# Performance work log

Measured on AMD Instinct MI355X. Metric: run time of the kernel, lower is better.

Reference implementation:

```python
import jax, jax.numpy as jnp
import numpy as np

B, D, H, DH, DFF = 2, 1024, 16, 64, 4096
NB, NR, S = 24, 8, 512
SCALE_DEPTH = 1.4
FSQ_DIM, FSQ_LEVELS = 32, 8
EPS = 1e-5


def rmsnorm(x, w):
    var = jnp.mean(x * x, axis=-1, keepdims=True)
    return x * jax.lax.rsqrt(var + EPS) * w


def rope_cos_sin(position):
    # position: [B] int -> cos/sin [B, DH/2]
    inv = 1.0 / (10000.0 ** (jnp.arange(0, DH, 2, dtype=jnp.float32) / DH))
    ang = position.astype(jnp.float32)[:, None] * inv[None, :]
    return jnp.cos(ang), jnp.sin(ang)


def apply_rope(x, cos, sin):
    # x: [B, H, 1, DH]
    x1, x2 = jnp.split(x, 2, axis=-1)
    c = cos[:, None, None, :]
    s = sin[:, None, None, :]
    return jnp.concatenate([x1 * c - x2 * s, x1 * s + x2 * c], axis=-1)


def run_lm(hidden, cache_k, cache_v, params, cos, sin, n_layers):
    # hidden [B,1,D]; cache_k/v [L,B,H,S,DH]; params: stacked per-layer weights.
    scale = SCALE_DEPTH / np.sqrt(n_layers)  # MuP residual scale
    inv_sqrt_dh = 1.0 / np.sqrt(DH)

    def body(h, xs):
        ln1, wq, wk, wv, wo, ln2, wg, wu, wd, ck, cv = xs
        res = h
        hn = rmsnorm(h, ln1)
        q = (hn @ wq).reshape(B, 1, H, DH).transpose(0, 2, 1, 3)
        k = (hn @ wk).reshape(B, 1, H, DH).transpose(0, 2, 1, 3)
        v = (hn @ wv).reshape(B, 1, H, DH).transpose(0, 2, 1, 3)
        q = apply_rope(q, cos, sin)
        k = apply_rope(k, cos, sin)
        nk = jnp.concatenate([ck, k], axis=2)  # [B,H,S+1,DH]
        nv = jnp.concatenate([cv, v], axis=2)
        att = jnp.einsum('bhqd,bhkd->bhqk', q, nk) * inv_sqrt_dh
        p = jax.nn.softmax(att, axis=-1)
        o = jnp.einsum('bhqk,bhkd->bhqd', p, nv).transpose(0, 2, 1, 3).reshape(B, 1, D) @ wo
        h = res + o * scale
        res = h
        hn = rmsnorm(h, ln2)
        mlp = (jax.nn.silu(hn @ wg) * (hn @ wu)) @ wd
        h = res + mlp * scale
        return h, (nk, nv)

    ln1, wq, wk, wv, wo, ln2, wg, wu, wd = params
    hidden, (nk, nv) = jax.lax.scan(
        body, hidden, (ln1, wq, wk, wv, wo, ln2, wg, wu, wd, cache_k, cache_v))
    return hidden, nk, nv


def fsq(x, w_in, w_out):
    # finite scalar quantization with straight-through rounding
    z = jnp.tanh(x @ w_in)
    half = (FSQ_LEVELS - 1) / 2.0
    zq = jnp.round(z * half) / half
    zq = z + jax.lax.stop_gradient(zq - z)
    return zq @ w_out


def _forward(position, embed, base_k, base_v, res_k, res_v,
             base_ln1, base_ln2, base_wq, base_wk, base_wv, base_wo,
             base_wg, base_wu, base_wd, base_norm,
             res_ln1, res_ln2, res_wq, res_wk, res_wv, res_wo,
             res_wg, res_wu, res_wd, res_norm,
             fsq_in, fsq_out, stop_proj_w, stop_proj_b, stop_head_w, stop_head_b):
    cos, sin = rope_cos_sin(position)
    hidden, bnk, bnv = run_lm(
        embed, base_k, base_v,
        (base_ln1, base_wq, base_wk, base_wv, base_wo, base_ln2, base_wg, base_wu, base_wd),
        cos, sin, NB)
    lm_hidden = rmsnorm(hidden, base_norm)
    lm_fsq = fsq(lm_hidden, fsq_in, fsq_out)
    stop_logit = jax.nn.silu(lm_hidden @ stop_proj_w + stop_proj_b) @ stop_head_w + stop_head_b
    res_in = lm_fsq + embed
    rh, rnk, rnv = run_lm(
        res_in, res_k, res_v,
        (res_ln1, res_wq, res_wk, res_wv, res_wo, res_ln2, res_wg, res_wu, res_wd),
        cos, sin, NR)
    rh = rmsnorm(rh, res_norm)
    return (lm_fsq, rh, stop_logit, bnk, bnv, rnk, rnv)


def setup_inputs() -> dict:
    key = jax.random.key(0)
    ks = iter(jax.random.split(key, 40))

    def p(shape, scale=0.02):
        return jax.random.normal(next(ks), shape, dtype=jnp.float32) * scale

    return {
        'embed': jax.random.normal(next(ks), (B, 1, D), jnp.float32),
        'position': jax.random.randint(next(ks), (B,), 0, S),
        'base_k': jax.random.normal(next(ks), (NB, B, H, S, DH), jnp.float32),
        'base_v': jax.random.normal(next(ks), (NB, B, H, S, DH), jnp.float32),
        'res_k': jax.random.normal(next(ks), (NR, B, H, S, DH), jnp.float32),
        'res_v': jax.random.normal(next(ks), (NR, B, H, S, DH), jnp.float32),
        'base_ln1': jnp.ones((NB, D), jnp.float32),
        'base_ln2': jnp.ones((NB, D), jnp.float32),
        'base_wq': p((NB, D, D)), 'base_wk': p((NB, D, D)),
        'base_wv': p((NB, D, D)), 'base_wo': p((NB, D, D)),
        'base_wg': p((NB, D, DFF)), 'base_wu': p((NB, D, DFF)), 'base_wd': p((NB, DFF, D)),
        'base_norm': jnp.ones((D,), jnp.float32),
        'res_ln1': jnp.ones((NR, D), jnp.float32),
        'res_ln2': jnp.ones((NR, D), jnp.float32),
        'res_wq': p((NR, D, D)), 'res_wk': p((NR, D, D)),
        'res_wv': p((NR, D, D)), 'res_wo': p((NR, D, D)),
        'res_wg': p((NR, D, DFF)), 'res_wu': p((NR, D, DFF)), 'res_wd': p((NR, DFF, D)),
        'res_norm': jnp.ones((D,), jnp.float32),
        'fsq_in': p((D, FSQ_DIM)), 'fsq_out': p((FSQ_DIM, D)),
        'stop_proj_w': p((D, D)), 'stop_proj_b': jnp.zeros((D,), jnp.float32),
        'stop_head_w': p((D, 1)), 'stop_head_b': jnp.zeros((1,), jnp.float32),
    }


def reference(embed, position, base_k, base_v, res_k, res_v,
              base_ln1, base_ln2, base_wq, base_wk, base_wv, base_wo,
              base_wg, base_wu, base_wd, base_norm,
              res_ln1, res_ln2, res_wq, res_wk, res_wv, res_wo,
              res_wg, res_wu, res_wd, res_norm,
              fsq_in, fsq_out, stop_proj_w, stop_proj_b, stop_head_w, stop_head_b):
    return _forward(position, embed, base_k, base_v, res_k, res_v,
                    base_ln1, base_ln2, base_wq, base_wk, base_wv, base_wo,
                    base_wg, base_wu, base_wd, base_norm,
                    res_ln1, res_ln2, res_wq, res_wk, res_wv, res_wo,
                    res_wg, res_wu, res_wd, res_norm,
                    fsq_in, fsq_out, stop_proj_w, stop_proj_b, stop_head_w, stop_head_b)
```

## Files before the change

kernel.cpp:

```cpp
#include <hip/hip_runtime.h>
#include <cmath>

#define D 1024
#define DFF 4096
#define NHEADS 16
#define DH 64
#define S_CACHE 512
#define SP1 513
#define NB_L 24
#define NR_L 8
#define NCH 17

#define WS_H      0
#define WS_H2     2048
#define WS_QKV    4096
#define WS_ATTN   102400
#define WS_OPROJ  139392
#define WS_GU     155776
#define WS_DOWN   286848
#define WS_SPROJ  303232

__device__ __forceinline__ float silu(float x) { return x / (1.f + expf(-x)); }

__device__ __forceinline__ void prologue_norm(
    const float* __restrict__ hbase,
    const float* __restrict__ part, int nks, float scale,
    const float* __restrict__ lnw,
    float (*hn)[D], float* __restrict__ hout)
{
  __shared__ float redw[4];
  const int t = threadIdx.x;
  const int b = t >> 7;
  const int i0 = (t & 127) * 8;
  const float4* hb4 = (const float4*)(hbase + b * D + i0);
  const float4 h0 = hb4[0], h1 = hb4[1];
  float acc[8] = {h0.x, h0.y, h0.z, h0.w, h1.x, h1.y, h1.z, h1.w};
  if (part != nullptr) {
    float s[8] = {0,0,0,0,0,0,0,0};
    for (int ks = 0; ks < nks; ++ks) {
      const float4* p4 = (const float4*)(part + (size_t)(ks * 2 + b) * D + i0);
      const float4 a = p4[0], c = p4[1];
      s[0]+=a.x; s[1]+=a.y; s[2]+=a.z; s[3]+=a.w;
      s[4]+=c.x; s[5]+=c.y; s[6]+=c.z; s[7]+=c.w;
    }
#pragma unroll
    for (int u = 0; u < 8; ++u) acc[u] += scale * s[u];
  }
  float ssq = 0.f;
#pragma unroll
  for (int u = 0; u < 8; ++u) ssq += acc[u] * acc[u];
#pragma unroll
  for (int off = 32; off; off >>= 1) ssq += __shfl_xor(ssq, off);
  if ((t & 63) == 0) redw[t >> 6] = ssq;
  __syncthreads();
  const float r = rsqrtf((redw[b * 2] + redw[b * 2 + 1]) * (1.f / D) + 1e-5f);
#pragma unroll
  for (int u = 0; u < 8; ++u) hn[b][i0 + u] = acc[u] * r * lnw[i0 + u];
  if (hout != nullptr && blockIdx.x == 0 && blockIdx.y == 0) {
    float4* o4 = (float4*)(hout + b * D + i0);
    o4[0] = make_float4(acc[0], acc[1], acc[2], acc[3]);
    o4[1] = make_float4(acc[4], acc[5], acc[6], acc[7]);
  }
  __syncthreads();
}

__global__ __launch_bounds__(256) void k_qkv(
    const float* __restrict__ hbase, const float* __restrict__ down_part,
    float* __restrict__ hout, const float* __restrict__ ln1,
    const float* __restrict__ wq, const float* __restrict__ wk,
    const float* __restrict__ wv,
    float* __restrict__ qkv_part, float scale, int has_prev)
{
  __shared__ float hn[2][D];
  __shared__ float redg[16][2][64];
  const int t = threadIdx.x;
  const int ks = blockIdx.x;
  const int cg = blockIdx.y;
  const int mat = cg >> 4;
  const int jbase = (cg & 15) * 64;
  const float* W = (mat == 0) ? wq : (mat == 1) ? wk : wv;
  const int jo4 = (t & 15) * 4;
  const int kp = t >> 4;
  const int ib = ks * 64 + kp * 4;
  float4 wbuf[4];
#pragma unroll
  for (int r = 0; r < 4; ++r)
    wbuf[r] = *(const float4*)(W + (size_t)(ib + r) * D + jbase + jo4);
  prologue_norm(hbase, has_prev ? down_part : nullptr, 8, scale, ln1, hn, hout);
  float a00=0,a01=0,a02=0,a03=0, a10=0,a11=0,a12=0,a13=0;
#pragma unroll
  for (int r = 0; r < 4; ++r) {
    const float x0 = hn[0][ib + r], x1 = hn[1][ib + r];
    a00 += wbuf[r].x*x0; a01 += wbuf[r].y*x0; a02 += wbuf[r].z*x0; a03 += wbuf[r].w*x0;
    a10 += wbuf[r].x*x1; a11 += wbuf[r].y*x1; a12 += wbuf[r].z*x1; a13 += wbuf[r].w*x1;
  }
  redg[kp][0][jo4+0]=a00; redg[kp][0][jo4+1]=a01; redg[kp][0][jo4+2]=a02; redg[kp][0][jo4+3]=a03;
  redg[kp][1][jo4+0]=a10; redg[kp][1][jo4+1]=a11; redg[kp][1][jo4+2]=a12; redg[kp][1][jo4+3]=a13;
  __syncthreads();
  if (t < 128) {
    const int b = t >> 6, jo = t & 63;
    float s = 0.f;
#pragma unroll
    for (int k2 = 0; k2 < 16; ++k2) s += redg[k2][b][jo];
    qkv_part[(size_t)((ks * 3 + mat) * 2 + b) * D + jbase + jo] = s;
  }
}

__global__ __launch_bounds__(256) void k_attn(
    const float* __restrict__ qkv_part, const int* __restrict__ position,
    const float* __restrict__ k_in, const float* __restrict__ v_in,
    float* __restrict__ k_out, float* __restrict__ v_out,
    float* __restrict__ attn_part)
{
  const int t = threadIdx.x;
  const int chunk = blockIdx.x;
  const int bh = blockIdx.y;
  const int b = bh >> 4, h = bh & 15;
  __shared__ float q[64];
  __shared__ float sc[32];
  __shared__ float red8[8][32];
  __shared__ float pvred[16][64];
  __shared__ float mlsh[2];
  __shared__ float kn[64], vn[64];
  const size_t row_in  = (size_t)bh * S_CACHE;
  const size_t row_out = (size_t)bh * SP1;
  const int pbase = (bh * NCH + chunk) * 68;

  if (chunk < 16) {
    const float4* ksrc = (const float4*)(k_in + (row_in + chunk * 32) * 64);
    float4*       kdst = (float4*)(k_out + (row_out + chunk * 32) * 64);
    const float4* vsrc = (const float4*)(v_in + (row_in + chunk * 32) * 64);
    float4*       vdst = (float4*)(v_out + (row_out + chunk * 32) * 64);
    const float4 kc0 = ksrc[t], kc1 = ksrc[t + 256];
    const float4 vc0 = vsrc[t], vc1 = vsrc[t + 256];
    kdst[t] = kc0; kdst[t + 256] = kc1;
    vdst[t] = vc0; vdst[t + 256] = vc1;
    if (t < 64) {
      float s = 0.f;
#pragma unroll
      for (int ks = 0; ks < 16; ++ks)
        s += qkv_part[(size_t)(ks * 6 + b) * D + h * 64 + t];
      q[t] = s;
    }
    __syncthreads();
    if (t < 32) {
      const float pos = (float)position[b];
      const float inv = expf(-(float)t * 0.28782313662425575f);
      const float ang = pos * inv;
      const float c = cosf(ang), sn = sinf(ang);
      const float x1 = q[t], x2 = q[t + 32];
      q[t]      = (x1 * c - x2 * sn) * 0.125f;
      q[t + 32] = (x1 * sn + x2 * c) * 0.125f;
    }
    __syncthreads();
    {
      const int key = t & 31, kp = t >> 5;
      const float* krow = k_in + (row_in + chunk * 32 + key) * 64 + kp * 8;
      const float4 k0 = *(const float4*)krow;
      const float4 k1 = *(const float4*)(krow + 4);
      const int d = kp * 8;
      float dp = k0.x*q[d] + k0.y*q[d+1] + k0.z*q[d+2] + k0.w*q[d+3]
               + k1.x*q[d+4] + k1.y*q[d+5] + k1.z*q[d+6] + k1.w*q[d+7];
      red8[kp][key] = dp;
    }
    __syncthreads();
    if (t < 32) {
      float score = 0.f;
#pragma unroll
      for (int k2 = 0; k2 < 8; ++k2) score += red8[k2][t];
      float m = score;
#pragma unroll
      for (int off = 16; off; off >>= 1) m = fmaxf(m, __shfl_xor(m, off));
      const float p = expf(score - m);
      float l = p;
#pragma unroll
      for (int off = 16; off; off >>= 1) l += __shfl_xor(l, off);
      sc[t] = p;
      if (t == 0) { mlsh[0] = m; mlsh[1] = l; }
    }
    __syncthreads();
    {
      const int d4 = (t & 15) * 4, sp = t >> 4;
      float ax = 0.f, ay = 0.f, az = 0.f, aw = 0.f;
#pragma unroll
      for (int r = 0; r < 2; ++r) {
        const int sl = sp * 2 + r;
        const float4 vv = *(const float4*)(v_in + (row_in + chunk * 32 + sl) * 64 + d4);
        const float p2 = sc[sl];
        ax += vv.x * p2; ay += vv.y * p2; az += vv.z * p2; aw += vv.w * p2;
      }
      pvred[sp][d4+0]=ax; pvred[sp][d4+1]=ay; pvred[sp][d4+2]=az; pvred[sp][d4+3]=aw;
    }
    __syncthreads();
    if (t < 64) {
      float a = 0.f;
#pragma unroll
      for (int s2 = 0; s2 < 16; ++s2) a += pvred[s2][t];
      attn_part[pbase + 2 + t] = a;
      if (t == 0) { attn_part[pbase + 0] = mlsh[0]; attn_part[pbase + 1] = mlsh[1]; }
    }
  } else {
    if (t < 64) {
      float skv = 0.f, svv = 0.f;
#pragma unroll
      for (int ks = 0; ks < 16; ++ks) {
        skv += qkv_part[(size_t)(ks * 6 + 2 + b) * D + h * 64 + t];
        svv += qkv_part[(size_t)(ks * 6 + 4 + b) * D + h * 64 + t];
      }
      kn[t] = skv; vn[t] = svv;
    }
    if (t < 64) {
      float s = 0.f;
#pragma unroll
      for (int ks = 0; ks < 16; ++ks)
        s += qkv_part[(size_t)(ks * 6 + b) * D + h * 64 + t];
      q[t] = s;
    }
    __syncthreads();
    if (t < 32) {
      const float pos = (float)position[b];
      const float inv = expf(-(float)t * 0.28782313662425575f);
      const float ang = pos * inv;
      const float c = cosf(ang), sn = sinf(ang);
      float x1 = kn[t], x2 = kn[t + 32];
      kn[t]      = x1 * c - x2 * sn;
      kn[t + 32] = x1 * sn + x2 * c;
      x1 = q[t]; x2 = q[t + 32];
      q[t]      = (x1 * c - x2 * sn) * 0.125f;
      q[t + 32] = (x1 * sn + x2 * c) * 0.125f;
    }
    __syncthreads();
    if (t < 64) {
      k_out[(row_out + S_CACHE) * 64 + t] = kn[t];
      v_out[(row_out + S_CACHE) * 64 + t] = vn[t];
      float dp = q[t] * kn[t];
#pragma unroll
      for (int off = 32; off; off >>= 1) dp += __shfl_xor(dp, off);
      attn_part[pbase + 2 + t] = vn[t];
      if (t == 0) { attn_part[pbase + 0] = dp; attn_part[pbase + 1] = 1.f; }
    }
  }
}

__global__ __launch_bounds__(256) void k_oproj(
    const float* __restrict__ attn_part, const float* __restrict__ wo,
    float* __restrict__ oproj_part)
{
  __shared__ float o[2][128];
  __shared__ float cw[2][2][NCH];
  __shared__ float redg[32][2][32];
  const int t = threadIdx.x;
  const int ks = blockIdx.x;
  const int cg = blockIdx.y;
  const int ibeg = ks * 128;
  const int jbase = cg * 32;
  const int jo4 = (t & 7) * 4;
  const int kp = t >> 3;
  float4 wbuf[4];
#pragma unroll
  for (int r = 0; r < 4; ++r)
    wbuf[r] = *(const float4*)(wo + (size_t)(ibeg + kp * 4 + r) * D + jbase + jo4);
  if (t < 4) {
    const int bb = t >> 1, hr = t & 1;
    const int hh = ks * 2 + hr;
    const int base = ((bb * 16 + hh) * NCH) * 68;
    float mg = -1e30f;
    for (int c = 0; c < NCH; ++c) mg = fmaxf(mg, attn_part[base + c * 68]);
    float lg = 0.f;
    float wloc[NCH];
    for (int c = 0; c < NCH; ++c) {
      const float w = expf(attn_part[base + c * 68] - mg);
      wloc[c] = w;
      lg += attn_part[base + c * 68 + 1] * w;
    }
    const float invl = 1.f / lg;
    for (int c = 0; c < NCH; ++c) cw[bb][hr][c] = wloc[c] * invl;
  }
  __syncthreads();
  {
    const int bb = t >> 7, ir = t & 127;
    const int i = ibeg + ir;
    const int hh = i >> 6, hr = hh - ks * 2, d = i & 63;
    float s = 0.f;
#pragma unroll
    for (int c = 0; c < NCH; ++c)
      s += attn_part[((bb * 16 + hh) * NCH + c) * 68 + 2 + d] * cw[bb][hr][c];
    o[bb][ir] = s;
  }
  __syncthreads();
  float a00=0,a01=0,a02=0,a03=0, a10=0,a11=0,a12=0,a13=0;
#pragma unroll
  for (int r = 0; r < 4; ++r) {
    const int ir = kp * 4 + r;
    const float x0 = o[0][ir], x1 = o[1][ir];
    a00 += wbuf[r].x*x0; a01 += wbuf[r].y*x0; a02 += wbuf[r].z*x0; a03 += wbuf[r].w*x0;
    a10 += wbuf[r].x*x1; a11 += wbuf[r].y*x1; a12 += wbuf[r].z*x1; a13 += wbuf[r].w*x1;
  }
  redg[kp][0][jo4+0]=a00; redg[kp][0][jo4+1]=a01; redg[kp][0][jo4+2]=a02; redg[kp][0][jo4+3]=a03;
  redg[kp][1][jo4+0]=a10; redg[kp][1][jo4+1]=a11; redg[kp][1][jo4+2]=a12; redg[kp][1][jo4+3]=a13;
  __syncthreads();
  if (t < 64) {
    const int b = t >> 5, jo = t & 31;
    float s = 0.f;
#pragma unroll
    for (int k2 = 0; k2 < 32; ++k2) s += redg[k2][b][jo];
    oproj_part[(size_t)(ks * 2 + b) * D + jbase + jo] = s;
  }
}

__global__ __launch_bounds__(256) void k_gateup(
    const float* __restrict__ hbase, const float* __restrict__ oproj_part,
    float* __restrict__ h2_out, const float* __restrict__ ln2,
    const float* __restrict__ wg, const float* __restrict__ wu,
    float* __restrict__ gu_part, float scale)
{
  __shared__ float hn[2][D];
  __shared__ float redg[16][4][64];
  const int t = threadIdx.x;
  const int ks = blockIdx.x;
  const int cg = blockIdx.y;
  const int jbase = cg * 64;
  const int jo4 = (t & 15) * 4;
  const int kp = t >> 4;
  const int ib = ks * 128 + kp * 8;
  float4 wgb[8];
#pragma unroll
  for (int r = 0; r < 8; ++r)
    wgb[r] = *(const float4*)(wg + (size_t)(ib + r) * DFF + jbase + jo4);
  prologue_norm(hbase, oproj_part, 8, scale, ln2, hn, h2_out);
  float g00=0,g01=0,g02=0,g03=0, g10=0,g11=0,g12=0,g13=0;
  float u00=0,u01=0,u02=0,u03=0, u10=0,u11=0,u12=0,u13=0;
#pragma unroll
  for (int r = 0; r < 8; ++r) {
    const float x0 = hn[0][ib + r], x1 = hn[1][ib + r];
    g00 += wgb[r].x*x0; g01 += wgb[r].y*x0; g02 += wgb[r].z*x0; g03 += wgb[r].w*x0;
    g10 += wgb[r].x*x1; g11 += wgb[r].y*x1; g12 += wgb[r].z*x1; g13 += wgb[r].w*x1;
  }
#pragma unroll
  for (int r = 0; r < 8; ++r) {
    const float4 c = *(const float4*)(wu + (size_t)(ib + r) * DFF + jbase + jo4);
    const float x0 = hn[0][ib + r], x1 = hn[1][ib + r];
    u00 += c.x*x0; u01 += c.y*x0; u02 += c.z*x0; u03 += c.w*x0;
    u10 += c.x*x1; u11 += c.y*x1; u12 += c.z*x1; u13 += c.w*x1;
  }
  redg[kp][0][jo4+0]=g00; redg[kp][0][jo4+1]=g01; redg[kp][0][jo4+2]=g02; redg[kp][0][jo4+3]=g03;
  redg[kp][1][jo4+0]=g10; redg[kp][1][jo4+1]=g11; redg[kp][1][jo4+2]=g12; redg[kp][1][jo4+3]=g13;
  redg[kp][2][jo4+0]=u00; redg[kp][2][jo4+1]=u01; redg[kp][2][jo4+2]=u02; redg[kp][2][jo4+3]=u03;
  redg[kp][3][jo4+0]=u10; redg[kp][3][jo4+1]=u11; redg[kp][3][jo4+2]=u12; redg[kp][3][jo4+3]=u13;
  __syncthreads();
  {
    const int sel = t >> 6;
    const int jo = t & 63;
    float s = 0.f;
#pragma unroll
    for (int k2 = 0; k2 < 16; ++k2) s += redg[k2][sel][jo];
    const int gm = sel >> 1, b = sel & 1;
    gu_part[(size_t)(ks * 4 + gm * 2 + b) * DFF + jbase + jo] = s;
  }
}

__global__ __launch_bounds__(256) void k_down(
    const float* __restrict__ gu_part, const float* __restrict__ wd,
    float* __restrict__ down_part)
{
  __shared__ float act[2][512];
  __shared__ float redg[32][2][32];
  const int t = threadIdx.x;
  const int ks = blockIdx.x;
  const int cg = blockIdx.y;
  const int ibeg = ks * 512;
  const int jbase = cg * 32;
  const int jo4 = (t & 7) * 4;
  const int kp = t >> 3;
  const int ib = kp * 16;
  float4 wbuf[8];
#pragma unroll
  for (int r = 0; r < 8; ++r)
    wbuf[r] = *(const float4*)(wd + (size_t)(ibeg + ib + r) * D + jbase + jo4);
#pragma unroll
  for (int u = 0; u < 4; ++u) {
    const int e = u * 256 + t;
    const int b = e >> 9, ir = e & 511;
    const int i = ibeg + ir;
    float g = 0.f, uu = 0.f;
#pragma unroll
    for (int k = 0; k < 8; ++k) {
      g  += gu_part[(size_t)(k * 4 + b) * DFF + i];
      uu += gu_part[(size_t)(k * 4 + 2 + b) * DFF + i];
    }
    act[b][ir] = silu(g) * uu;
  }
  __syncthreads();
  float a00=0,a01=0,a02=0,a03=0, a10=0,a11=0,a12=0,a13=0;
#pragma unroll
  for (int r = 0; r < 8; ++r) {
    const float x0 = act[0][ib + r], x1 = act[1][ib + r];
    a00 += wbuf[r].x*x0; a01 += wbuf[r].y*x0; a02 += wbuf[r].z*x0; a03 += wbuf[r].w*x0;
    a10 += wbuf[r].x*x1; a11 += wbuf[r].y*x1; a12 += wbuf[r].z*x1; a13 += wbuf[r].w*x1;
  }
#pragma unroll
  for (int r = 8; r < 16; ++r) {
    const float4 w = *(const float4*)(wd + (size_t)(ibeg + ib + r) * D + jbase + jo4);
    const float x0 = act[0][ib + r], x1 = act[1][ib + r];
    a00 += w.x*x0; a01 += w.y*x0; a02 += w.z*x0; a03 += w.w*x0;
    a10 += w.x*x1; a11 += w.y*x1; a12 += w.z*x1; a13 += w.w*x1;
  }
  redg[kp][0][jo4+0]=a00; redg[kp][0][jo4+1]=a01; redg[kp][0][jo4+2]=a02; redg[kp][0][jo4+3]=a03;
  redg[kp][1][jo4+0]=a10; redg[kp][1][jo4+1]=a11; redg[kp][1][jo4+2]=a12; redg[kp][1][jo4+3]=a13;
  __syncthreads();
  if (t < 64) {
    const int b = t >> 5, jo = t & 31;
    float s = 0.f;
#pragma unroll
    for (int k2 = 0; k2 < 32; ++k2) s += redg[k2][b][jo];
    down_part[(size_t)(ks * 2 + b) * D + jbase + jo] = s;
  }
}

__global__ __launch_bounds__(256) void k_heads(
    const float* __restrict__ hbase, const float* __restrict__ down_part,
    const float* __restrict__ normw, const float* __restrict__ wsp,
    float* __restrict__ sproj_part,
    const float* __restrict__ fsq_in, const float* __restrict__ fsq_out,
    const float* __restrict__ embed,
    float* __restrict__ out_fsq, float* __restrict__ h_res, float scale)
{
  __shared__ float hn[2][D];
  const int t = threadIdx.x;
  const int bid = blockIdx.x;
  if (bid < 128) {
    __shared__ float redg[16][2][64];
    const int ks = bid >> 4, cg = bid & 15;
    const int jbase = cg * 64;
    const int jo4 = (t & 15) * 4;
    const int kp = t >> 4;
    const int ib = ks * 128 + kp * 8;
    float4 wbuf[8];
#pragma unroll
    for (int r = 0; r < 8; ++r)
      wbuf[r] = *(const float4*)(wsp + (size_t)(ib + r) * D + jbase + jo4);
    prologue_norm(hbase, down_part, 8, scale, normw, hn, nullptr);
    float a00=0,a01=0,a02=0,a03=0, a10=0,a11=0,a12=0,a13=0;
#pragma unroll
    for (int r = 0; r < 8; ++r) {
      const float x0 = hn[0][ib + r], x1 = hn[1][ib + r];
      a00 += wbuf[r].x*x0; a01 += wbuf[r].y*x0; a02 += wbuf[r].z*x0; a03 += wbuf[r].w*x0;
      a10 += wbuf[r].x*x1; a11 += wbuf[r].y*x1; a12 += wbuf[r].z*x1; a13 += wbuf[r].w*x1;
    }
    redg[kp][0][jo4+0]=a00; redg[kp][0][jo4+1]=a01; redg[kp][0][jo4+2]=a02; redg[kp][0][jo4+3]=a03;
    redg[kp][1][jo4+0]=a10; redg[kp][1][jo4+1]=a11; redg[kp][1][jo4+2]=a12; redg[kp][1][jo4+3]=a13;
    __syncthreads();
    if (t < 128) {
      const int b = t >> 6, jo = t & 63;
      float s = 0.f;
#pragma unroll
      for (int k2 = 0; k2 < 16; ++k2) s += redg[k2][b][jo];
      sproj_part[(size_t)(ks * 2 + b) * D + jbase + jo] = s;
    }
  } else {
    __shared__ float zred[4][2][32];
    __shared__ float zq[2][32];
    prologue_norm(hbase, down_part, 8, scale, normw, hn, nullptr);
    {
      const int c = t & 31, b = (t >> 5) & 1, kp = t >> 6;
      float s = 0.f;
      for (int i = kp * 256; i < kp * 256 + 256; ++i) s += hn[b][i] * fsq_in[i * 32 + c];
      zred[kp][b][c] = s;
    }
    __syncthreads();
    if (t < 64) {
      const int b = t >> 5, c = t & 31;
      float z = zred[0][b][c] + zred[1][b][c] + zred[2][b][c] + zred[3][b][c];
      z = tanhf(z);
      zq[b][c] = rintf(z * 3.5f) / 3.5f;
    }
    __syncthreads();
    if (t < 128) {
      const int b = t >> 6, jo = t & 63;
      const int j = (bid - 128) * 64 + jo;
      float s = 0.f;
#pragma unroll
      for (int c = 0; c < 32; ++c) s += zq[b][c] * fsq_out[c * D + j];
      out_fsq[b * D + j] = s;
      h_res[b * D + j] = s + embed[b * D + j];
    }
  }
}

__global__ __launch_bounds__(256) void k_stophead(
    const float* __restrict__ sproj_part, const float* __restrict__ bvec,
    const float* __restrict__ hw, const float* __restrict__ hb,
    float* __restrict__ out_stop)
{
  const int t = threadIdx.x;
  float acc0 = 0.f, acc1 = 0.f;
  for (int j = t; j < D; j += 256) {
    float v0 = bvec[j], v1 = bvec[j];
#pragma unroll
    for (int ks = 0; ks < 8; ++ks) {
      v0 += sproj_part[(ks * 2 + 0) * D + j];
      v1 += sproj_part[(ks * 2 + 1) * D + j];
    }
    acc0 += silu(v0) * hw[j];
    acc1 += silu(v1) * hw[j];
  }
  __shared__ float red[256];
  red[t] = acc0;
  __syncthreads();
  for (int s = 128; s > 0; s >>= 1) { if (t < s) red[t] += red[t + s]; __syncthreads(); }
  if (t == 0) out_stop[0] = red[0] + hb[0];
  __syncthreads();
  red[t] = acc1;
  __syncthreads();
  for (int s = 128; s > 0; s >>= 1) { if (t < s) red[t] += red[t + s]; __syncthreads(); }
  if (t == 0) out_stop[1] = red[0] + hb[0];
}

__global__ __launch_bounds__(256) void k_final(
    const float* __restrict__ hbase, const float* __restrict__ down_part,
    const float* __restrict__ normw, float* __restrict__ out_rh, float scale)
{
  __shared__ float hn[2][D];
  prologue_norm(hbase, down_part, 8, scale, normw, hn, nullptr);
  const int t = threadIdx.x;
  const int b = t >> 7;
  const int i0 = (t & 127) * 8;
#pragma unroll
  for (int u = 0; u < 8; ++u) out_rh[b * D + i0 + u] = hn[b][i0 + u];
}

extern "C" void kernel_launch(void* const* d_in, const int* in_sizes, int n_in,
                              void* d_out, int out_size, void* d_ws, size_t ws_size,
                              hipStream_t stream) {
  const float* embed      = (const float*)d_in[0];
  const int*   position   = (const int*)d_in[1];
  const float* base_k     = (const float*)d_in[2];
  const float* base_v     = (const float*)d_in[3];
  const float* res_k      = (const float*)d_in[4];
  const float* res_v      = (const float*)d_in[5];
  const float* base_ln1   = (const float*)d_in[6];
  const float* base_ln2   = (const float*)d_in[7];
  const float* base_wq    = (const float*)d_in[8];
  const float* base_wk    = (const float*)d_in[9];
  const float* base_wv    = (const float*)d_in[10];
  const float* base_wo    = (const float*)d_in[11];
  const float* base_wg    = (const float*)d_in[12];
  const float* base_wu    = (const float*)d_in[13];
  const float* base_wd    = (const float*)d_in[14];
  const float* base_norm  = (const float*)d_in[15];
  const float* res_ln1    = (const float*)d_in[16];
  const float* res_ln2    = (const float*)d_in[17];
  const float* res_wq     = (const float*)d_in[18];
  const float* res_wk     = (const float*)d_in[19];
  const float* res_wv     = (const float*)d_in[20];
  const float* res_wo     = (const float*)d_in[21];
  const float* res_wg     = (const float*)d_in[22];
  const float* res_wu     = (const float*)d_in[23];
  const float* res_wd     = (const float*)d_in[24];
  const float* res_norm   = (const float*)d_in[25];
  const float* fsq_in     = (const float*)d_in[26];
  const float* fsq_out    = (const float*)d_in[27];
  const float* stop_proj_w = (const float*)d_in[28];
  const float* stop_proj_b = (const float*)d_in[29];
  const float* stop_head_w = (const float*)d_in[30];
  const float* stop_head_b = (const float*)d_in[31];

  float* out = (float*)d_out;
  float* ws = (float*)d_ws;
  float* W_h     = ws + WS_H;
  float* W_h2    = ws + WS_H2;
  float* W_qkv   = ws + WS_QKV;
  float* W_attn  = ws + WS_ATTN;
  float* W_oproj = ws + WS_OPROJ;
  float* W_gu    = ws + WS_GU;
  float* W_down  = ws + WS_DOWN;
  float* W_sproj = ws + WS_SPROJ;

  const size_t cacheL_in  = (size_t)2 * NHEADS * S_CACHE * DH;
  const size_t cacheL_out = (size_t)2 * NHEADS * SP1 * DH;
  float* out_fsq  = out;
  float* out_rh   = out + 2048;
  float* out_stop = out + 4096;
  float* out_bnk  = out + 4098;
  float* out_bnv  = out_bnk + (size_t)NB_L * cacheL_out;
  float* out_rnk  = out_bnv + (size_t)NB_L * cacheL_out;
  float* out_rnv  = out_rnk + (size_t)NR_L * cacheL_out;

  const float scaleB = 1.4f / sqrtf((float)NB_L);
  const float scaleR = 1.4f / sqrtf((float)NR_L);

  auto run_layer = [&](const float* hbase, float* hout,
                       const float* ln1, const float* ln2,
                       const float* wq, const float* wk, const float* wv,
                       const float* wo, const float* wg, const float* wu,
                       const float* wd,
                       const float* kin, const float* vin,
                       float* kout, float* vout,
                       float scale, int has_prev) {
    k_qkv<<<dim3(16, 48), 256, 0, stream>>>(hbase, W_down, hout, ln1,
                                            wq, wk, wv, W_qkv, scale, has_prev);
    k_attn<<<dim3(NCH, 32), 256, 0, stream>>>(W_qkv, position, kin, vin, kout, vout, W_attn);
    k_oproj<<<dim3(8, 32), 256, 0, stream>>>(W_attn, wo, W_oproj);
    k_gateup<<<dim3(8, 64), 256, 0, stream>>>(W_h, W_oproj, W_h2, ln2, wg, wu, W_gu, scale);
    k_down<<<dim3(8, 32), 256, 0, stream>>>(W_gu, wd, W_down);
  };

  for (int l = 0; l < NB_L; ++l) {
    run_layer(l == 0 ? embed : W_h2, W_h,
              base_ln1 + (size_t)l * D, base_ln2 + (size_t)l * D,
              base_wq + (size_t)l * D * D, base_wk + (size_t)l * D * D,
              base_wv + (size_t)l * D * D, base_wo + (size_t)l * D * D,
              base_wg + (size_t)l * D * DFF, base_wu + (size_t)l * D * DFF,
              base_wd + (size_t)l * DFF * D,
              base_k + (size_t)l * cacheL_in, base_v + (size_t)l * cacheL_in,
              out_bnk + (size_t)l * cacheL_out, out_bnv + (size_t)l * cacheL_out,
              scaleB, l > 0);
  }

  k_heads<<<144, 256, 0, stream>>>(W_h2, W_down, base_norm, stop_proj_w, W_sproj,
                                   fsq_in, fsq_out, embed, out_fsq, W_h, scaleB);
  k_stophead<<<1, 256, 0, stream>>>(W_sproj, stop_proj_b, stop_head_w, stop_head_b, out_stop);

  for (int l = 0; l < NR_L; ++l) {
    run_layer(l == 0 ? W_h : W_h2, l == 0 ? nullptr : W_h,
              res_ln1 + (size_t)l * D, res_ln2 + (size_t)l * D,
              res_wq + (size_t)l * D * D, res_wk + (size_t)l * D * D,
              res_wv + (size_t)l * D * D, res_wo + (size_t)l * D * D,
              res_wg + (size_t)l * D * DFF, res_wu + (size_t)l * D * DFF,
              res_wd + (size_t)l * DFF * D,
              res_k + (size_t)l * cacheL_in, res_v + (size_t)l * cacheL_in,
              out_rnk + (size_t)l * cacheL_out, out_rnv + (size_t)l * cacheL_out,
              scaleR, l > 0);
  }

  k_final<<<1, 256, 0, stream>>>(W_h2, W_down, res_norm, out_rh, scaleR);
}
```

Measured before the change: 1.185 ms.

## Fold new-token attention into last cache chunk and use nontemporal KV copies

The separate 17th attention block that handled only the freshly projected key/value token is removed, and its work moves into chunk 15. That block now computes the new key's score, merges it into the chunk's softmax max and sum, and adds its weighted value. The cache copy to the output KV buffers now uses nontemporal stores. This cuts a mostly idle block per head and shrinks the partials that the output projection must combine, at the cost of extra divergent work in one block per head.

```diff
diff --git a/kernel.cpp b/kernel.cpp
--- a/kernel.cpp
+++ b/kernel.cpp
@@ -9,7 +9,9 @@
 #define SP1 513
 #define NB_L 24
 #define NR_L 8
-#define NCH 17
+#define NCH 16
+
+typedef float v4f __attribute__((ext_vector_type(4)));
 
 #define WS_H      0
 #define WS_H2     2048
@@ -20,7 +22,7 @@
 #define WS_DOWN   286848
 #define WS_SPROJ  303232
 
-__device__ __forceinline__ float silu(float x) { return x / (1.f + expf(-x)); }
+__device__ __forceinline__ float silu_f(float x){ return x/(1.f+expf(-x)); }
 
 __device__ __forceinline__ void prologue_norm(
     const float* __restrict__ hbase,
@@ -116,129 +118,129 @@
   const int chunk = blockIdx.x;
   const int bh = blockIdx.y;
   const int b = bh >> 4, h = bh & 15;
-  __shared__ float q[64];
-  __shared__ float sc[32];
+  const bool hasNew = (chunk == 15);
+  __shared__ float q[64], kn[64], vn[64];
+  __shared__ float sc[33];
   __shared__ float red8[8][32];
   __shared__ float pvred[16][64];
-  __shared__ float mlsh[2];
-  __shared__ float kn[64], vn[64];
+  __shared__ float msl[3];
   const size_t row_in  = (size_t)bh * S_CACHE;
   const size_t row_out = (size_t)bh * SP1;
   const int pbase = (bh * NCH + chunk) * 68;
 
-  if (chunk < 16) {
-    const float4* ksrc = (const float4*)(k_in + (row_in + chunk * 32) * 64);
-    float4*       kdst = (float4*)(k_out + (row_out + chunk * 32) * 64);
-    const float4* vsrc = (const float4*)(v_in + (row_in + chunk * 32) * 64);
-    float4*       vdst = (float4*)(v_out + (row_out + chunk * 32) * 64);
-    const float4 kc0 = ksrc[t], kc1 = ksrc[t + 256];
-    const float4 vc0 = vsrc[t], vc1 = vsrc[t + 256];
-    kdst[t] = kc0; kdst[t + 256] = kc1;
-    vdst[t] = vc0; vdst[t + 256] = vc1;
-    if (t < 64) {
-      float s = 0.f;
-#pragma unroll
-      for (int ks = 0; ks < 16; ++ks)
-        s += qkv_part[(size_t)(ks * 6 + b) * D + h * 64 + t];
-      q[t] = s;
-    }
-    __syncthreads();
+  {
+    const v4f* ksrc = (const v4f*)(k_in + (row_in + chunk * 32) * 64);
+    const v4f* vsrc = (const v4f*)(v_in + (row_in + chunk * 32) * 64);
+    v4f* kdst = (v4f*)(k_out + (row_out + chunk * 32) * 64);
+    v4f* vdst = (v4f*)(v_out + (row_out + chunk * 32) * 64);
+    const v4f kc0 = ksrc[t], kc1 = ksrc[t + 256];
+    const v4f vc0 = vsrc[t], vc1 = vsrc[t + 256];
+    __builtin_nontemporal_store(kc0, &kdst[t]);
+    __builtin_nontemporal_store(kc1, &kdst[t + 256]);
+    __builtin_nontemporal_store(vc0, &vdst[t]);
+    __builtin_nontemporal_store(vc1, &vdst[t + 256]);
+  }
+  if (t < 64) {
+    float s = 0.f;
+#pragma unroll
+    for (int ks = 0; ks < 16; ++ks)
+      s += qkv_part[(size_t)(ks * 6 + b) * D + h * 64 + t];
+    q[t] = s;
+  } else if (hasNew && t < 128) {
+    const int u = t - 64;
+    float s = 0.f;
+#pragma unroll
+    for (int ks = 0; ks < 16; ++ks)
+      s += qkv_part[(size_t)(ks * 6 + 2 + b) * D + h * 64 + u];
+    kn[u] = s;
+  } else if (hasNew && t < 192) {
+    const int u = t - 128;
+    float s = 0.f;
+#pragma unroll
+    for (int ks = 0; ks < 16; ++ks)
+      s += qkv_part[(size_t)(ks * 6 + 4 + b) * D + h * 64 + u];
+    vn[u] = s;
+  }
+  __syncthreads();
+  {
+    const float pos = (float)position[b];
     if (t < 32) {
-      const float pos = (float)position[b];
       const float inv = expf(-(float)t * 0.28782313662425575f);
       const float ang = pos * inv;
       const float c = cosf(ang), sn = sinf(ang);
       const float x1 = q[t], x2 = q[t + 32];
       q[t]      = (x1 * c - x2 * sn) * 0.125f;
       q[t + 32] = (x1 * sn + x2 * c) * 0.125f;
-    }
-    __syncthreads();
-    {
-      const int key = t & 31, kp = t >> 5;
-      const float* krow = k_in + (row_in + chunk * 32 + key) * 64 + kp * 8;
-      const float4 k0 = *(const float4*)krow;
-      const float4 k1 = *(const float4*)(krow + 4);
-      const int d = kp * 8;
-      float dp = k0.x*q[d] + k0.y*q[d+1] + k0.z*q[d+2] + k0.w*q[d+3]
-               + k1.x*q[d+4] + k1.y*q[d+5] + k1.z*q[d+6] + k1.w*q[d+7];
-      red8[kp][key] = dp;
-    }
-    __syncthreads();
-    if (t < 32) {
-      float score = 0.f;
-#pragma unroll
-      for (int k2 = 0; k2 < 8; ++k2) score += red8[k2][t];
-      float m = score;
-#pragma unroll
-      for (int off = 16; off; off >>= 1) m = fmaxf(m, __shfl_xor(m, off));
-      const float p = expf(score - m);
-      float l = p;
-#pragma unroll
-      for (int off = 16; off; off >>= 1) l += __shfl_xor(l, off);
-      sc[t] = p;
-      if (t == 0) { mlsh[0] = m; mlsh[1] = l; }
-    }
-    __syncthreads();
-    {
-      const int d4 = (t & 15) * 4, sp = t >> 4;
-      float ax = 0.f, ay = 0.f, az = 0.f, aw = 0.f;
-#pragma unroll
-      for (int r = 0; r < 2; ++r) {
-        const int sl = sp * 2 + r;
-        const float4 vv = *(const float4*)(v_in + (row_in + chunk * 32 + sl) * 64 + d4);
-        const float p2 = sc[sl];
-        ax += vv.x * p2; ay += vv.y * p2; az += vv.z * p2; aw += vv.w * p2;
-      }
-      pvred[sp][d4+0]=ax; pvred[sp][d4+1]=ay; pvred[sp][d4+2]=az; pvred[sp][d4+3]=aw;
-    }
-    __syncthreads();
-    if (t < 64) {
-      float a = 0.f;
-#pragma unroll
-      for (int s2 = 0; s2 < 16; ++s2) a += pvred[s2][t];
-      attn_part[pbase + 2 + t] = a;
-      if (t == 0) { attn_part[pbase + 0] = mlsh[0]; attn_part[pbase + 1] = mlsh[1]; }
-    }
-  } else {
-    if (t < 64) {
-      float skv = 0.f, svv = 0.f;
-#pragma unroll
-      for (int ks = 0; ks < 16; ++ks) {
-        skv += qkv_part[(size_t)(ks * 6 + 2 + b) * D + h * 64 + t];
-        svv += qkv_part[(size_t)(ks * 6 + 4 + b) * D + h * 64 + t];
-      }
-      kn[t] = skv; vn[t] = svv;
-    }
-    if (t < 64) {
-      float s = 0.f;
-#pragma unroll
-      for (int ks = 0; ks < 16; ++ks)
-        s += qkv_part[(size_t)(ks * 6 + b) * D + h * 64 + t];
-      q[t] = s;
-    }
-    __syncthreads();
-    if (t < 32) {
-      const float pos = (float)position[b];
-      const float inv = expf(-(float)t * 0.28782313662425575f);
+    } else if (hasNew && t < 64) {
+      const int u = t - 32;
+      const float inv = expf(-(float)u * 0.28782313662425575f);
       const float ang = pos * inv;
       const float c = cosf(ang), sn = sinf(ang);
-      float x1 = kn[t], x2 = kn[t + 32];
-      kn[t]      = x1 * c - x2 * sn;
-      kn[t + 32] = x1 * sn + x2 * c;
-      x1 = q[t]; x2 = q[t + 32];
-      q[t]      = (x1 * c - x2 * sn) * 0.125f;
-      q[t + 32] = (x1 * sn + x2 * c) * 0.125f;
-    }
-    __syncthreads();
-    if (t < 64) {
-      k_out[(row_out + S_CACHE) * 64 + t] = kn[t];
-      v_out[(row_out + S_CACHE) * 64 + t] = vn[t];
-      float dp = q[t] * kn[t];
-#pragma unroll
-      for (int off = 32; off; off >>= 1) dp += __shfl_xor(dp, off);
-      attn_part[pbase + 2 + t] = vn[t];
-      if (t == 0) { attn_part[pbase + 0] = dp; attn_part[pbase + 1] = 1.f; }
-    }
+      const float x1 = kn[u], x2 = kn[u + 32];
+      kn[u]      = x1 * c - x2 * sn;
+      kn[u + 32] = x1 * sn + x2 * c;
+    }
+  }
+  __syncthreads();
+  if (hasNew && t < 64) {
+    k_out[(row_out + S_CACHE) * 64 + t] = kn[t];
+    v_out[(row_out + S_CACHE) * 64 + t] = vn[t];
+    float dp = q[t] * kn[t];
+#pragma unroll
+    for (int off = 32; off; off >>= 1) dp += __shfl_xor(dp, off);
+    if (t == 0) msl[0] = dp;
+  }
+  {
+    const int key = t & 31, kp = t >> 5;
+    const float* krow = k_in + (row_in + chunk * 32 + key) * 64 + kp * 8;
+    const float4 k0 = *(const float4*)krow;
+    const float4 k1 = *(const float4*)(krow + 4);
+    const int d = kp * 8;
+    float dp = k0.x*q[d] + k0.y*q[d+1] + k0.z*q[d+2] + k0.w*q[d+3]
+             + k1.x*q[d+4] + k1.y*q[d+5] + k1.z*q[d+6] + k1.w*q[d+7];
+    red8[kp][key] = dp;
+  }
+  __syncthreads();
+  if (t < 32) {
+    float score = 0.f;
+#pragma unroll
+    for (int k2 = 0; k2 < 8; ++k2) score += red8[k2][t];
+    float m = score;
+#pragma unroll
+    for (int off = 16; off; off >>= 1) m = fmaxf(m, __shfl_xor(m, off));
+    const float nsc = hasNew ? msl[0] : -1e30f;
+    m = fmaxf(m, nsc);
+    const float p = expf(score - m);
+    float l = p;
+#pragma unroll
+    for (int off = 16; off; off >>= 1) l += __shfl_xor(l, off);
+    sc[t] = p;
+    if (t == 0) {
+      const float pn = hasNew ? expf(nsc - m) : 0.f;
+      sc[32] = pn; msl[1] = m; msl[2] = l + pn;
+    }
+  }
+  __syncthreads();
+  {
+    const int d4 = (t & 15) * 4, sp = t >> 4;
+    float ax = 0.f, ay = 0.f, az = 0.f, aw = 0.f;
+#pragma unroll
+    for (int r = 0; r < 2; ++r) {
+      const int sl = sp * 2 + r;
+      const float4 vv = *(const float4*)(v_in + (row_in + chunk * 32 + sl) * 64 + d4);
+      const float p2 = sc[sl];
+      ax += vv.x * p2; ay += vv.y * p2; az += vv.z * p2; aw += vv.w * p2;
+    }
+    pvred[sp][d4+0]=ax; pvred[sp][d4+1]=ay; pvred[sp][d4+2]=az; pvred[sp][d4+3]=aw;
+  }
+  __syncthreads();
+  if (t < 64) {
+    float a = 0.f;
+#pragma unroll
+    for (int s2 = 0; s2 < 16; ++s2) a += pvred[s2][t];
+    if (hasNew) a += sc[32] * vn[t];
+    attn_part[pbase + 2 + t] = a;
+    if (t == 0) { attn_part[pbase + 0] = msl[1]; attn_part[pbase + 1] = msl[2]; }
   }
 }
 
@@ -388,7 +390,7 @@
       g  += gu_part[(size_t)(k * 4 + b) * DFF + i];
       uu += gu_part[(size_t)(k * 4 + 2 + b) * DFF + i];
     }
-    act[b][ir] = silu(g) * uu;
+    act[b][ir] = silu_f(g) * uu;
   }
   __syncthreads();
   float a00=0,a01=0,a02=0,a03=0, a10=0,a11=0,a12=0,a13=0;
@@ -501,8 +503,8 @@
       v0 += sproj_part[(ks * 2 + 0) * D + j];
       v1 += sproj_part[(ks * 2 + 1) * D + j];
     }
-    acc0 += silu(v0) * hw[j];
-    acc1 += silu(v1) * hw[j];
+    acc0 += silu_f(v0) * hw[j];
+    acc1 += silu_f(v1) * hw[j];
   }
   __shared__ float red[256];
   red[t] = acc0;
```

Result: faster. 1.162 ms (-2.0%).
